# Kernel tuning notes

Hardware: AMD Instinct MI355X
Metric: run time of the kernel (lower is better)

## Reference

```python
import jax, jax.numpy as jnp
import numpy as np

N_HEADS = 8
D_MODEL = 256
N_NODES = 4096


def setup_inputs() -> dict:
    key = jax.random.key(0)
    ks = jax.random.split(key, 8)
    s = 1.0 / np.sqrt(D_MODEL)
    return {
        "input_Q": jax.random.normal(ks[0], (N_NODES, D_MODEL), jnp.float32),
        "input_K": jax.random.normal(ks[1], (N_NODES, D_MODEL), jnp.float32),
        "input_V": jax.random.normal(ks[2], (N_NODES, D_MODEL), jnp.float32),
        "adj_matrix": jax.random.uniform(ks[3], (N_NODES, N_NODES), jnp.float32),
        "dist_matrix": jax.random.uniform(ks[4], (N_NODES, N_NODES), jnp.float32) * 4.0,
        "W_Q": jax.random.normal(ks[5], (D_MODEL, D_MODEL), jnp.float32) * s,
        "W_K": jax.random.normal(ks[6], (D_MODEL, D_MODEL), jnp.float32) * s,
        "W_V": jax.random.normal(ks[7], (D_MODEL, D_MODEL), jnp.float32) * s,
    }


def rescale_distance_matrix(dist):
    c = 1.0
    return (c + jnp.exp(c)) / (c + jnp.exp(c - dist))


def reference(input_Q, input_K, input_V, adj_matrix, dist_matrix, W_Q, W_K, W_V):
    N, d_model = input_Q.shape
    H = N_HEADS
    dh = d_model // H  # d_k in the torch code (K.size(2) after transpose)
    # Linear (no bias): x @ W^T, then view [N, H, dh] -> [H, N, dh]
    Q = (input_Q @ W_Q.T).reshape(N, H, dh).transpose(1, 0, 2)
    K = (input_K @ W_K.T).reshape(N, H, dh).transpose(1, 0, 2)
    V = (input_V @ W_V.T).reshape(N, H, dh).transpose(1, 0, 2)
    # When both adj and dist are given, the torch code overwrites the adj path;
    # effective scores = ReLU(Q K^T) @ rescale(dist) / sqrt(dh). adj_matrix is dead code.
    qk = jnp.einsum('hnd,hmd->hnm', Q, K)  # [H, N, N]
    scores = jnp.einsum('hnm,mp->hnp', jax.nn.relu(qk), rescale_distance_matrix(dist_matrix)) / jnp.sqrt(
        jnp.asarray(dh, Q.dtype))
    attn = jax.nn.softmax(scores, axis=-1)
    context = jnp.einsum('hnm,hmd->hnd', attn, V)  # [H, N, dh]
    return context.transpose(1, 0, 2).reshape(N, d_model)
```

## Files before the change

### kernel.cpp

```cpp
#include <hip/hip_runtime.h>
#include <stdint.h>

#define NN_ 4096
#define DM_ 256

typedef unsigned short ushort_t;
typedef __bf16 bf16x8 __attribute__((ext_vector_type(8)));
typedef _Float16 f16x8 __attribute__((ext_vector_type(8)));
typedef float f32x4 __attribute__((ext_vector_type(4)));

__device__ __forceinline__ unsigned short f32_to_bf16(float x) {
  unsigned int u = __float_as_uint(x);
  unsigned int r = u + 0x7FFFu + ((u >> 16) & 1u);
  return (unsigned short)(r >> 16);
}
__device__ __forceinline__ float bf16_to_f32(unsigned short h) {
  return __uint_as_float(((unsigned int)h) << 16);
}

__device__ __forceinline__ void async_cp16(const void* g, void* l) {
  auto gp = reinterpret_cast<__attribute__((address_space(1))) unsigned int*>(
      reinterpret_cast<uintptr_t>(g));
  auto lp = reinterpret_cast<__attribute__((address_space(3))) unsigned int*>(
      reinterpret_cast<uintptr_t>(l));
  __builtin_amdgcn_global_load_lds(gp, lp, 16, 0, 0);
}

__global__ __launch_bounds__(256) void rescale_kernel(const float* __restrict__ dist,
                                                      _Float16* __restrict__ Rth,
                                                      _Float16* __restrict__ Rtl) {
  __shared__ float tile[64][65];
  const int m0 = blockIdx.y * 64;
  const int p0 = blockIdx.x * 64;
  const int t = threadIdx.x;
  const int c = t & 63;
  const int rg = t >> 6;
  const float C = 3.718281828459045f;
  for (int i = 0; i < 16; i++) {
    int ml = rg * 16 + i;
    float d = dist[(size_t)(m0 + ml) * NN_ + p0 + c];
    tile[c][ml] = C / (1.0f + expf(1.0f - d));
  }
  __syncthreads();
  for (int i = 0; i < 16; i++) {
    int pl = rg * 16 + i;
    float v = tile[pl][c];
    _Float16 hv = (_Float16)v;
    size_t o = (size_t)(p0 + pl) * NN_ + m0 + c;
    Rth[o] = hv;
    Rtl[o] = (_Float16)(v - (float)hv);
  }
}

__global__ __launch_bounds__(256) void proj_kernel(const float* __restrict__ X,
                                                   const float* __restrict__ W,
                                                   float* __restrict__ Of,
                                                   ushort_t* __restrict__ O1,
                                                   ushort_t* __restrict__ O2) {
  __shared__ float Xs[64][33];
  __shared__ float Ws[64][33];
  const int m0 = blockIdx.y * 64;
  const int n0 = blockIdx.x * 64;
  const int t = threadIdx.x;
  const int tm = t >> 4, tn = t & 15;
  float acc[4][4] = {};
  for (int k0 = 0; k0 < DM_; k0 += 32) {
    for (int q = 0; q < 2; q++) {
      int id = t + q * 256;
      int row = id >> 3;
      int c4 = (id & 7) * 4;
      float4 vx = *(const float4*)&X[(size_t)(m0 + row) * DM_ + k0 + c4];
      Xs[row][c4] = vx.x; Xs[row][c4 + 1] = vx.y; Xs[row][c4 + 2] = vx.z; Xs[row][c4 + 3] = vx.w;
      float4 vw = *(const float4*)&W[(size_t)(n0 + row) * DM_ + k0 + c4];
      Ws[row][c4] = vw.x; Ws[row][c4 + 1] = vw.y; Ws[row][c4 + 2] = vw.z; Ws[row][c4 + 3] = vw.w;
    }
    __syncthreads();
    for (int kk = 0; kk < 32; kk++) {
      float xi[4], wj[4];
      for (int i = 0; i < 4; i++) xi[i] = Xs[tm * 4 + i][kk];
      for (int j = 0; j < 4; j++) wj[j] = Ws[tn * 4 + j][kk];
      for (int i = 0; i < 4; i++)
        for (int j = 0; j < 4; j++) acc[i][j] += xi[i] * wj[j];
    }
    __syncthreads();
  }
  for (int i = 0; i < 4; i++)
    for (int j = 0; j < 4; j++) {
      size_t o = (size_t)(m0 + tm * 4 + i) * DM_ + n0 + tn * 4 + j;
      float v = acc[i][j];
      if (Of != nullptr) Of[o] = v;
      if (O1 != nullptr) {
        unsigned short hh = f32_to_bf16(v);
        O1[o] = hh;
        O2[o] = f32_to_bf16(v - bf16_to_f32(hh));
      }
    }
}

__global__ __launch_bounds__(256) void qk_kernel(const ushort_t* __restrict__ Q1,
                                                 const ushort_t* __restrict__ Q2,
                                                 const ushort_t* __restrict__ K1,
                                                 const ushort_t* __restrict__ K2,
                                                 _Float16* __restrict__ Ah,
                                                 _Float16* __restrict__ Al,
                                                 float* __restrict__ rowMax, int h) {
  const int n0 = blockIdx.y * 64;
  const int m0 = blockIdx.x * 64;
  const int t = threadIdx.x;
  if (blockIdx.x == 0 && blockIdx.y == 0) {
    for (int i = t; i < NN_; i += 256) rowMax[i] = 0.f;
  }
  const int wave = t >> 6, lane = t & 63;
  const int wm = wave >> 1, wn = wave & 1;
  const int r16 = lane & 15, quad = lane >> 4;
  const int ho = h * 32 + quad * 8;
  f32x4 acc[2][2] = {};
  bf16x8 a1[2], a2[2], b1[2], b2[2];
  for (int i = 0; i < 2; i++) {
    int row = n0 + wm * 32 + i * 16 + r16;
    a1[i] = *(const bf16x8*)&Q1[(size_t)row * DM_ + ho];
    a2[i] = *(const bf16x8*)&Q2[(size_t)row * DM_ + ho];
  }
  for (int j = 0; j < 2; j++) {
    int col = m0 + wn * 32 + j * 16 + r16;
    b1[j] = *(const bf16x8*)&K1[(size_t)col * DM_ + ho];
    b2[j] = *(const bf16x8*)&K2[(size_t)col * DM_ + ho];
  }
  for (int i = 0; i < 2; i++)
    for (int j = 0; j < 2; j++) {
      acc[i][j] = __builtin_amdgcn_mfma_f32_16x16x32_bf16(a1[i], b1[j], acc[i][j], 0, 0, 0);
      acc[i][j] = __builtin_amdgcn_mfma_f32_16x16x32_bf16(a1[i], b2[j], acc[i][j], 0, 0, 0);
      acc[i][j] = __builtin_amdgcn_mfma_f32_16x16x32_bf16(a2[i], b1[j], acc[i][j], 0, 0, 0);
    }
  const float scale = 0.17677669529663688f;
  for (int i = 0; i < 2; i++)
    for (int j = 0; j < 2; j++)
      for (int r = 0; r < 4; r++) {
        int row = n0 + wm * 32 + i * 16 + quad * 4 + r;
        int col = m0 + wn * 32 + j * 16 + r16;
        float w = acc[i][j][r] * scale;
        w = w > 0.f ? w : 0.f;
        _Float16 hh = (_Float16)w;
        size_t o = (size_t)row * NN_ + col;
        Ah[o] = hh;
        Al[o] = (_Float16)(w - (float)hh);
      }
}

__global__ __launch_bounds__(256) void sgemm_kernel(const _Float16* __restrict__ Ah,
                                                    const _Float16* __restrict__ Rth,
                                                    _Float16* __restrict__ Sh,
                                                    float* __restrict__ rowMax) {
  __shared__ _Float16 sA[128 * 64], sB[128 * 64];
  const int m0 = blockIdx.y * 128;
  const int p0 = blockIdx.x * 128;
  const int t = threadIdx.x;
  const int wave = t >> 6, lane = t & 63;
  const int wm = wave >> 1, wn = wave & 1;
  const int r16 = lane & 15, quad = lane >> 4;
  const int srow = lane >> 3;
  const int cg = (lane & 7) ^ srow;
  f32x4 acc[4][4] = {};
  for (int k0 = 0; k0 < NN_; k0 += 64) {
    for (int tt = 0; tt < 4; tt++) {
      int rl = wave * 32 + tt * 8;
      async_cp16(&Ah[(size_t)(m0 + rl + srow) * NN_ + k0 + cg * 8], &sA[rl * 64]);
      async_cp16(&Rth[(size_t)(p0 + rl + srow) * NN_ + k0 + cg * 8], &sB[rl * 64]);
    }
    __syncthreads();
    f16x8 af[4][2], bg[4][2];
    for (int i = 0; i < 4; i++) {
      int r = wm * 64 + i * 16 + r16;
      int s0 = quad ^ (r & 7);
      int s1 = (4 + quad) ^ (r & 7);
      af[i][0] = *(const f16x8*)&sA[r * 64 + s0 * 8];
      af[i][1] = *(const f16x8*)&sA[r * 64 + s1 * 8];
    }
    for (int j = 0; j < 4; j++) {
      int r = wn * 64 + j * 16 + r16;
      int s0 = quad ^ (r & 7);
      int s1 = (4 + quad) ^ (r & 7);
      bg[j][0] = *(const f16x8*)&sB[r * 64 + s0 * 8];
      bg[j][1] = *(const f16x8*)&sB[r * 64 + s1 * 8];
    }
    for (int i = 0; i < 4; i++)
      for (int j = 0; j < 4; j++) {
        acc[i][j] = __builtin_amdgcn_mfma_f32_16x16x32_f16(af[i][0], bg[j][0], acc[i][j], 0, 0, 0);
        acc[i][j] = __builtin_amdgcn_mfma_f32_16x16x32_f16(af[i][1], bg[j][1], acc[i][j], 0, 0, 0);
      }
    __syncthreads();
  }
  for (int i = 0; i < 4; i++)
    for (int r = 0; r < 4; r++) {
      float mv = fmaxf(fmaxf(acc[i][0][r], acc[i][1][r]),
                       fmaxf(acc[i][2][r], acc[i][3][r]));
      for (int off = 1; off < 16; off <<= 1) mv = fmaxf(mv, __shfl_xor(mv, off, 64));
      if (r16 == 0) {
        int row = m0 + wm * 64 + i * 16 + quad * 4 + r;
        atomicMax((unsigned int*)&rowMax[row], __float_as_uint(mv));
      }
    }
  for (int i = 0; i < 4; i++)
    for (int j = 0; j < 4; j++)
      for (int r = 0; r < 4; r++) {
        int row = m0 + wm * 64 + i * 16 + quad * 4 + r;
        int col = p0 + wn * 64 + j * 16 + r16;
        Sh[(size_t)row * NN_ + col] = (_Float16)acc[i][j][r];
      }
}

__global__ __launch_bounds__(256) void refine_kernel(const _Float16* __restrict__ Sh,
                                                     const float* __restrict__ rowMax,
                                                     const _Float16* __restrict__ Ah,
                                                     const _Float16* __restrict__ Al,
                                                     const _Float16* __restrict__ Rth,
                                                     const _Float16* __restrict__ Rtl,
                                                     const float* __restrict__ Vf,
                                                     float* __restrict__ out, int h) {
  __shared__ int plist[64];
  __shared__ int cnt;
  __shared__ float mW[4], lW[4];
  __shared__ float oW[4][32];
  const int t = threadIdx.x;
  const int wave = t >> 6, lane = t & 63;
  const int n = blockIdx.x;
  if (t == 0) cnt = 0;
  __syncthreads();
  const float thr = rowMax[n] - 16.0f;
  const _Float16* srow = Sh + (size_t)n * NN_;
  for (int q = 0; q < 2; q++) {
    int it = wave * 2 + q;
    f16x8 v = *(const f16x8*)&srow[it * 512 + lane * 8];
#pragma unroll
    for (int e = 0; e < 8; e++) {
      if ((float)v[e] > thr) {
        int idx = atomicAdd(&cnt, 1);
        if (idx < 64) plist[idx] = it * 512 + lane * 8 + e;
      }
    }
  }
  __syncthreads();
  int C = cnt;
  if (C > 64) C = 64;
  const _Float16* arh = Ah + (size_t)n * NN_;
  const _Float16* arl = Al + (size_t)n * NN_;
  float mcur = -1e30f, lsum = 0.f, oacc = 0.f;
  for (int j = wave; j < C; j += 4) {
    int p = plist[j];
    const _Float16* rh = Rth + (size_t)p * NN_;
    const _Float16* rl = Rtl + (size_t)p * NN_;
    float d = 0.f;
#pragma unroll
    for (int it = 0; it < 8; it++) {
      int m = it * 512 + lane * 8;
      f16x8 a8 = *(const f16x8*)&arh[m];
      f16x8 l8 = *(const f16x8*)&arl[m];
      f16x8 c8 = *(const f16x8*)&rh[m];
      f16x8 e8 = *(const f16x8*)&rl[m];
#pragma unroll
      for (int e = 0; e < 8; e++)
        d += ((float)a8[e] + (float)l8[e]) * ((float)c8[e] + (float)e8[e]);
    }
    for (int off = 32; off > 0; off >>= 1) d += __shfl_xor(d, off, 64);
    float vval = (lane < 32) ? Vf[(size_t)p * DM_ + h * 32 + lane] : 0.f;
    float nm = fmaxf(mcur, d);
    float alpha = __expf(mcur - nm);
    float w = __expf(d - nm);
    lsum = lsum * alpha + w;
    oacc = oacc * alpha + w * vval;
    mcur = nm;
  }
  if (lane == 0) { mW[wave] = mcur; lW[wave] = lsum; }
  if (lane < 32) oW[wave][lane] = oacc;
  __syncthreads();
  if (wave == 0 && lane < 32) {
    float M = fmaxf(fmaxf(mW[0], mW[1]), fmaxf(mW[2], mW[3]));
    float l = 0.f, o = 0.f;
#pragma unroll
    for (int w = 0; w < 4; w++) {
      float al = __expf(mW[w] - M);
      l += lW[w] * al;
      o += oW[w][lane] * al;
    }
    out[(size_t)n * DM_ + h * 32 + lane] = o / l;
  }
}

extern "C" void kernel_launch(void* const* d_in, const int* in_sizes, int n_in,
                              void* d_out, int out_size, void* d_ws, size_t ws_size,
                              hipStream_t stream) {
  const float* inQ = (const float*)d_in[0];
  const float* inK = (const float*)d_in[1];
  const float* inV = (const float*)d_in[2];
  const float* dist = (const float*)d_in[4];
  const float* WQ = (const float*)d_in[5];
  const float* WK = (const float*)d_in[6];
  const float* WV = (const float*)d_in[7];
  float* out = (float*)d_out;

  const size_t ND = (size_t)NN_ * DM_;
  const size_t NSQ = (size_t)NN_ * NN_;
  float* Vf = (float*)d_ws;
  ushort_t* Q1 = (ushort_t*)(Vf + ND);
  ushort_t* Q2 = Q1 + ND;
  ushort_t* K1 = Q2 + ND;
  ushort_t* K2 = K1 + ND;
  _Float16* Rth = (_Float16*)(K2 + ND);
  _Float16* Rtl = Rth + NSQ;
  _Float16* Ah = Rtl + NSQ;
  _Float16* Al = Ah + NSQ;
  _Float16* Sh = Al + NSQ;
  float* rowMax = (float*)(Sh + NSQ);

  rescale_kernel<<<dim3(64, 64), 256, 0, stream>>>(dist, Rth, Rtl);
  proj_kernel<<<dim3(4, 64), 256, 0, stream>>>(inQ, WQ, (float*)nullptr, Q1, Q2);
  proj_kernel<<<dim3(4, 64), 256, 0, stream>>>(inK, WK, (float*)nullptr, K1, K2);
  proj_kernel<<<dim3(4, 64), 256, 0, stream>>>(inV, WV, Vf, (ushort_t*)nullptr, (ushort_t*)nullptr);
  for (int h = 0; h < 8; h++) {
    qk_kernel<<<dim3(64, 64), 256, 0, stream>>>(Q1, Q2, K1, K2, Ah, Al, rowMax, h);
    sgemm_kernel<<<dim3(32, 32), 256, 0, stream>>>(Ah, Rth, Sh, rowMax);
    refine_kernel<<<NN_, 256, 0, stream>>>(Sh, rowMax, Ah, Al, Rth, Rtl, Vf, out, h);
  }
}
```

Measured before the change: 2.243 ms.

## Rewrite sgemm as 256x256 tile, 8-wave double-buffered pipelined kernel

Replaces the 128x128 single-buffered fp16 GEMM (A @ rescaled dist) with a 256x256 tile per 512-thread block. Shared memory is double-buffered and loads for the next k-step are interleaved with MFMA work across four quadrant phases, using explicit vmcnt waits, barriers and setprio. A block-index swizzle is added for L2 locality. The aim is to hide global load latency and raise arithmetic intensity, at the cost of high register pressure (128 accumulators per thread), 128KB of LDS, and only 256 blocks per launch.

```diff
diff --git a/kernel.cpp b/kernel.cpp
--- a/kernel.cpp
+++ b/kernel.cpp
@@ -147,66 +147,149 @@
       }
 }
 
-__global__ __launch_bounds__(256) void sgemm_kernel(const _Float16* __restrict__ Ah,
-                                                    const _Float16* __restrict__ Rth,
-                                                    _Float16* __restrict__ Sh,
-                                                    float* __restrict__ rowMax) {
-  __shared__ _Float16 sA[128 * 64], sB[128 * 64];
-  const int m0 = blockIdx.y * 128;
-  const int p0 = blockIdx.x * 128;
-  const int t = threadIdx.x;
-  const int wave = t >> 6, lane = t & 63;
-  const int wm = wave >> 1, wn = wave & 1;
+template <int SLOT>
+__device__ __forceinline__ void stage_half(const _Float16* __restrict__ Ah,
+                                           const _Float16* __restrict__ Rth,
+                                           int m0, int p0, _Float16* sAY, _Float16* sBY,
+                                           int tn, int wave, int srow, int cg) {
+  const _Float16* src = (SLOT == 0 || SLOT == 3) ? Ah : Rth;
+  const int gr0 = ((SLOT == 0 || SLOT == 3) ? m0 : p0) + ((SLOT >= 2) ? 128 : 0);
+  _Float16* dst = ((SLOT == 0 || SLOT == 3) ? sAY : sBY) + ((SLOT >= 2) ? 128 * 64 : 0);
+  const int k0 = tn * 64;
+#pragma unroll
+  for (int q = 0; q < 2; q++) {
+    const int rl = wave * 16 + q * 8;
+    async_cp16(&src[(size_t)(gr0 + rl + srow) * NN_ + k0 + cg * 8], dst + rl * 64);
+  }
+}
+
+template <int P>
+__device__ __forceinline__ void phase_reads(const _Float16* sAX, const _Float16* sBX,
+                                            int wr, int wc, int r16, int quad,
+                                            f16x8 (&af)[4][2], f16x8 (&bg)[2][2]) {
+  constexpr int qm = P >> 1, qn = P & 1;
+#pragma unroll
+  for (int i = 0; i < 4; i++) {
+    int ar = qm * 128 + wr * 64 + i * 16 + r16;
+    const _Float16* base = sAX + ar * 64;
+    int x = ar & 7;
+    af[i][0] = *(const f16x8*)(base + (quad ^ x) * 8);
+    af[i][1] = *(const f16x8*)(base + ((4 + quad) ^ x) * 8);
+  }
+#pragma unroll
+  for (int j = 0; j < 2; j++) {
+    int br = qn * 128 + wc * 32 + j * 16 + r16;
+    const _Float16* base = sBX + br * 64;
+    int x = br & 7;
+    bg[j][0] = *(const f16x8*)(base + (quad ^ x) * 8);
+    bg[j][1] = *(const f16x8*)(base + ((4 + quad) ^ x) * 8);
+  }
+}
+
+template <int P>
+__device__ __forceinline__ void phase_mac(f32x4 (&acc)[4][4][2],
+                                          f16x8 (&af)[4][2], f16x8 (&bg)[2][2]) {
+#pragma unroll
+  for (int i = 0; i < 4; i++)
+#pragma unroll
+    for (int j = 0; j < 2; j++) {
+      acc[P][i][j] = __builtin_amdgcn_mfma_f32_16x16x32_f16(af[i][0], bg[j][0], acc[P][i][j], 0, 0, 0);
+      acc[P][i][j] = __builtin_amdgcn_mfma_f32_16x16x32_f16(af[i][1], bg[j][1], acc[P][i][j], 0, 0, 0);
+    }
+}
+
+__global__ __launch_bounds__(512, 2) void sgemm_kernel(const _Float16* __restrict__ Ah,
+                                                       const _Float16* __restrict__ Rth,
+                                                       _Float16* __restrict__ Sh,
+                                                       float* __restrict__ rowMax) {
+  __shared__ _Float16 sA[2][256 * 64];
+  __shared__ _Float16 sB[2][256 * 64];
+  const int b = blockIdx.x;
+  const int swz = (b & 7) * 32 + (b >> 3);
+  const int m0 = (swz >> 4) * 256;
+  const int p0 = (swz & 15) * 256;
+  const int tid = threadIdx.x;
+  const int wave = tid >> 6, lane = tid & 63;
+  const int wr = wave >> 2, wc = wave & 3;
   const int r16 = lane & 15, quad = lane >> 4;
   const int srow = lane >> 3;
   const int cg = (lane & 7) ^ srow;
-  f32x4 acc[4][4] = {};
-  for (int k0 = 0; k0 < NN_; k0 += 64) {
-    for (int tt = 0; tt < 4; tt++) {
-      int rl = wave * 32 + tt * 8;
-      async_cp16(&Ah[(size_t)(m0 + rl + srow) * NN_ + k0 + cg * 8], &sA[rl * 64]);
-      async_cp16(&Rth[(size_t)(p0 + rl + srow) * NN_ + k0 + cg * 8], &sB[rl * 64]);
-    }
-    __syncthreads();
-    f16x8 af[4][2], bg[4][2];
-    for (int i = 0; i < 4; i++) {
-      int r = wm * 64 + i * 16 + r16;
-      int s0 = quad ^ (r & 7);
-      int s1 = (4 + quad) ^ (r & 7);
-      af[i][0] = *(const f16x8*)&sA[r * 64 + s0 * 8];
-      af[i][1] = *(const f16x8*)&sA[r * 64 + s1 * 8];
-    }
-    for (int j = 0; j < 4; j++) {
-      int r = wn * 64 + j * 16 + r16;
-      int s0 = quad ^ (r & 7);
-      int s1 = (4 + quad) ^ (r & 7);
-      bg[j][0] = *(const f16x8*)&sB[r * 64 + s0 * 8];
-      bg[j][1] = *(const f16x8*)&sB[r * 64 + s1 * 8];
-    }
+
+  f32x4 acc[4][4][2] = {};
+
+  stage_half<0>(Ah, Rth, m0, p0, sA[0], sB[0], 0, wave, srow, cg);
+  stage_half<1>(Ah, Rth, m0, p0, sA[0], sB[0], 0, wave, srow, cg);
+  stage_half<2>(Ah, Rth, m0, p0, sA[0], sB[0], 0, wave, srow, cg);
+  stage_half<3>(Ah, Rth, m0, p0, sA[0], sB[0], 0, wave, srow, cg);
+  asm volatile("s_waitcnt vmcnt(4)" ::: "memory");
+  asm volatile("s_barrier" ::: "memory");
+
+#define PHASE(P, VMC)                                                              \
+  {                                                                                \
+    f16x8 af[4][2], bg[2][2];                                                      \
+    phase_reads<P>(sA[X], sB[X], wr, wc, r16, quad, af, bg);                       \
+    stage_half<P>(Ah, Rth, m0, p0, sA[Y], sB[Y], tt + 1, wave, srow, cg);          \
+    asm volatile("s_waitcnt vmcnt(" #VMC ")" ::: "memory");                        \
+    asm volatile("s_barrier" ::: "memory");                                        \
+    __builtin_amdgcn_s_setprio(1);                                                 \
+    phase_mac<P>(acc, af, bg);                                                     \
+    __builtin_amdgcn_s_setprio(0);                                                 \
+    asm volatile("s_barrier" ::: "memory");                                        \
+  }
+
+  for (int tt = 0; tt < 63; ++tt) {
+    const int X = tt & 1, Y = X ^ 1;
+    PHASE(0, 4)
+    PHASE(1, 4)
+    PHASE(2, 6)
+    PHASE(3, 4)
+  }
+#undef PHASE
+
+  asm volatile("s_waitcnt vmcnt(0)" ::: "memory");
+  asm volatile("s_barrier" ::: "memory");
+  {
+    f16x8 af[4][2], bg[2][2];
+    phase_reads<0>(sA[1], sB[1], wr, wc, r16, quad, af, bg);
+    phase_mac<0>(acc, af, bg);
+    phase_reads<1>(sA[1], sB[1], wr, wc, r16, quad, af, bg);
+    phase_mac<1>(acc, af, bg);
+    phase_reads<2>(sA[1], sB[1], wr, wc, r16, quad, af, bg);
+    phase_mac<2>(acc, af, bg);
+    phase_reads<3>(sA[1], sB[1], wr, wc, r16, quad, af, bg);
+    phase_mac<3>(acc, af, bg);
+  }
+
+#pragma unroll
+  for (int qm = 0; qm < 2; qm++)
+#pragma unroll
     for (int i = 0; i < 4; i++)
-      for (int j = 0; j < 4; j++) {
-        acc[i][j] = __builtin_amdgcn_mfma_f32_16x16x32_f16(af[i][0], bg[j][0], acc[i][j], 0, 0, 0);
-        acc[i][j] = __builtin_amdgcn_mfma_f32_16x16x32_f16(af[i][1], bg[j][1], acc[i][j], 0, 0, 0);
+#pragma unroll
+      for (int r = 0; r < 4; r++) {
+        float mv = acc[qm * 2][i][0][r];
+        mv = fmaxf(mv, acc[qm * 2][i][1][r]);
+        mv = fmaxf(mv, acc[qm * 2 + 1][i][0][r]);
+        mv = fmaxf(mv, acc[qm * 2 + 1][i][1][r]);
+        for (int off = 1; off < 16; off <<= 1) mv = fmaxf(mv, __shfl_xor(mv, off, 64));
+        if (r16 == 0) {
+          int row = m0 + qm * 128 + wr * 64 + i * 16 + quad * 4 + r;
+          atomicMax((unsigned int*)&rowMax[row], __float_as_uint(mv));
+        }
       }
-    __syncthreads();
-  }
-  for (int i = 0; i < 4; i++)
-    for (int r = 0; r < 4; r++) {
-      float mv = fmaxf(fmaxf(acc[i][0][r], acc[i][1][r]),
-                       fmaxf(acc[i][2][r], acc[i][3][r]));
-      for (int off = 1; off < 16; off <<= 1) mv = fmaxf(mv, __shfl_xor(mv, off, 64));
-      if (r16 == 0) {
-        int row = m0 + wm * 64 + i * 16 + quad * 4 + r;
-        atomicMax((unsigned int*)&rowMax[row], __float_as_uint(mv));
-      }
-    }
-  for (int i = 0; i < 4; i++)
-    for (int j = 0; j < 4; j++)
-      for (int r = 0; r < 4; r++) {
-        int row = m0 + wm * 64 + i * 16 + quad * 4 + r;
-        int col = p0 + wn * 64 + j * 16 + r16;
-        Sh[(size_t)row * NN_ + col] = (_Float16)acc[i][j][r];
-      }
+#pragma unroll
+  for (int p = 0; p < 4; p++) {
+    const int qm = p >> 1, qn = p & 1;
+#pragma unroll
+    for (int i = 0; i < 4; i++)
+#pragma unroll
+      for (int j = 0; j < 2; j++)
+#pragma unroll
+        for (int r = 0; r < 4; r++) {
+          int row = m0 + qm * 128 + wr * 64 + i * 16 + quad * 4 + r;
+          int col = p0 + qn * 128 + wc * 32 + j * 16 + r16;
+          Sh[(size_t)row * NN_ + col] = (_Float16)acc[p][i][j][r];
+        }
+  }
 }
 
 __global__ __launch_bounds__(256) void refine_kernel(const _Float16* __restrict__ Sh,
@@ -318,7 +401,7 @@
   proj_kernel<<<dim3(4, 64), 256, 0, stream>>>(inV, WV, Vf, (ushort_t*)nullptr, (ushort_t*)nullptr);
   for (int h = 0; h < 8; h++) {
     qk_kernel<<<dim3(64, 64), 256, 0, stream>>>(Q1, Q2, K1, K2, Ah, Al, rowMax, h);
-    sgemm_kernel<<<dim3(32, 32), 256, 0, stream>>>(Ah, Rth, Sh, rowMax);
+    sgemm_kernel<<<dim3(256), dim3(512), 0, stream>>>(Ah, Rth, Sh, rowMax);
     refine_kernel<<<NN_, 256, 0, stream>>>(Sh, rowMax, Ah, Al, Rth, Rtl, Vf, out, h);
   }
 }
```

After: 1.999 ms. 1.12x faster.
